# Optimization experiments

Hardware: AMD Instinct MI355X
Metric: run time of the kernel (lower is better)

## Reference

```python
import jax, jax.numpy as jnp
import numpy as np

N = 50000          # nodes
E = 1_600_000      # edges (before self-loops)
F_IN = 256
HID = 32
HEADS = 4
OUT = 64
NEG_SLOPE = 0.2


def setup_inputs() -> dict:
    key = jax.random.key(0)
    ks = jax.random.split(key, 10)
    x = jax.random.normal(ks[0], (N, F_IN), dtype=jnp.float32)
    edge_index = jax.random.randint(ks[1], (2, E), 0, N, dtype=jnp.int64)
    # layer 1: input_dim -> hidden*heads
    W1 = jax.random.normal(ks[2], (F_IN, HEADS * HID), dtype=jnp.float32) / np.sqrt(F_IN)
    att_src1 = jax.random.normal(ks[3], (HEADS, HID), dtype=jnp.float32) / np.sqrt(HID)
    att_dst1 = jax.random.normal(ks[4], (HEADS, HID), dtype=jnp.float32) / np.sqrt(HID)
    b1 = jnp.zeros((HEADS * HID,), dtype=jnp.float32)
    # layer 2: hidden*heads -> out, 1 head, concat=False
    W2 = jax.random.normal(ks[5], (HEADS * HID, OUT), dtype=jnp.float32) / np.sqrt(HEADS * HID)
    att_src2 = jax.random.normal(ks[6], (1, OUT), dtype=jnp.float32) / np.sqrt(OUT)
    att_dst2 = jax.random.normal(ks[7], (1, OUT), dtype=jnp.float32) / np.sqrt(OUT)
    b2 = jnp.zeros((OUT,), dtype=jnp.float32)
    return {"x": x, "edge_index": edge_index, "W1": W1, "att_src1": att_src1,
            "att_dst1": att_dst1, "b1": b1, "W2": W2, "att_src2": att_src2,
            "att_dst2": att_dst2, "b2": b2}


def gat_layer(x, src, dst, W, a_src, a_dst, bias, heads, out_dim, concat):
    n = x.shape[0]
    h = (x @ W).reshape(n, heads, out_dim)              # [N,H,C]
    # per-node attention logits
    al_src = jnp.sum(h * a_src[None], axis=-1)          # [N,H]
    al_dst = jnp.sum(h * a_dst[None], axis=-1)          # [N,H]
    e = al_src[src] + al_dst[dst]                       # [E',H]
    e = jax.nn.leaky_relu(e, NEG_SLOPE)
    # segment softmax over incoming edges of each dst node
    emax = jax.ops.segment_max(e, dst, num_segments=n)  # [N,H]
    ee = jnp.exp(e - emax[dst])
    denom = jax.ops.segment_sum(ee, dst, num_segments=n)
    alpha = ee / denom[dst]                             # [E',H]
    msg = h[src] * alpha[:, :, None]                    # [E',H,C]
    out = jax.ops.segment_sum(msg, dst, num_segments=n)  # [N,H,C]
    if concat:
        out = out.reshape(n, heads * out_dim)
    else:
        out = out.mean(axis=1)
    return out + bias


def reference(x, edge_index, W1, att_src1, att_dst1, b1, W2, att_src2, att_dst2, b2):
    # add self-loops (PyG GATConv default)
    loop = jnp.arange(N, dtype=edge_index.dtype)
    src = jnp.concatenate([edge_index[0], loop])
    dst = jnp.concatenate([edge_index[1], loop])
    # eval mode: dropout(p=0.5) is identity
    h = gat_layer(x, src, dst, W1, att_src1, att_dst1, b1, HEADS, HID, True)
    h = jax.nn.elu(h)
    out = gat_layer(h, src, dst, W2, att_src2, att_dst2, b2, 1, OUT, False)
    return out
```

## Files before the change

kernel.cpp:

```cpp
#include <hip/hip_runtime.h>
#include <hip/hip_bf16.h>
#include <hip/hip_fp16.h>
#include <math.h>

#define NNODES 50000
#define NEDGES 1600000
#define ETOT   (NEDGES + NNODES)
#define F_INN  256
#define NEG_SLOPE 0.2f
#define NBUCK  782
#define BCAP   2624
#define CNBLK  256
#define CBT    1024

__global__ __launch_bounds__(128) void detect_kernel(const unsigned int* __restrict__ ei,
                                                     int* __restrict__ flag) {
    __shared__ int nz;
    if (threadIdx.x == 0) nz = 0;
    __syncthreads();
    unsigned int v = ei[2 * threadIdx.x + 1];
    if (v != 0u) nz = 1;
    __syncthreads();
    if (threadIdx.x == 0) *flag = nz;
}

__device__ __forceinline__ void load_edge(const void* ei, bool is32, int i, int& s, int& d) {
    if (i < NEDGES) {
        if (is32) {
            const int* p = (const int*)ei;
            s = p[i]; d = p[NEDGES + i];
        } else {
            const long long* p = (const long long*)ei;
            s = (int)p[i]; d = (int)p[NEDGES + i];
        }
    } else {
        s = i - NEDGES; d = s;
    }
}

__global__ __launch_bounds__(CBT) void convert_kernel(const void* __restrict__ ei,
                                                      const int* __restrict__ flag,
                                                      int* __restrict__ bcnt,
                                                      int2* __restrict__ bpair) {
    __shared__ int hist[NBUCK];
    __shared__ int base[NBUCK];
    const int t = threadIdx.x;
    const int chunk = (ETOT + CNBLK - 1) / CNBLK;
    const int i0 = blockIdx.x * chunk;
    const int i1 = min(i0 + chunk, ETOT);
    for (int k = t; k < NBUCK; k += CBT) hist[k] = 0;
    __syncthreads();
    const bool is32 = (*flag) != 0;
    for (int i = i0 + t; i < i1; i += CBT) {
        int s, d; load_edge(ei, is32, i, s, d);
        atomicAdd(&hist[d >> 6], 1);
    }
    __syncthreads();
    for (int k = t; k < NBUCK; k += CBT) {
        int c = hist[k];
        base[k] = c ? atomicAdd(&bcnt[k], c) : 0;
        hist[k] = 0;
    }
    __syncthreads();
    for (int i = i0 + t; i < i1; i += CBT) {
        int s, d; load_edge(ei, is32, i, s, d);
        int b = d >> 6;
        int pos = base[b] + atomicAdd(&hist[b], 1);
        bpair[(size_t)b * BCAP + pos] = make_int2(s, d);
    }
}

__global__ __launch_bounds__(256) void deg_kernel(const int2* __restrict__ bpair,
                                                  const int* __restrict__ bcnt,
                                                  int* __restrict__ deg) {
    __shared__ int cnt[64];
    const int b = blockIdx.x, t = threadIdx.x;
    if (t < 64) cnt[t] = 0;
    __syncthreads();
    const int n = bcnt[b];
    const int2* bp = bpair + (size_t)b * BCAP;
    for (int i = t; i < n; i += 256) atomicAdd(&cnt[bp[i].y & 63], 1);
    __syncthreads();
    int node = (b << 6) + t;
    if (t < 64 && node < NNODES) deg[node] = cnt[t];
}

__global__ __launch_bounds__(1024) void scan_kernel(const int* __restrict__ deg,
                                                    int* __restrict__ rowptr) {
    const int CH = 49;
    __shared__ int wsum[16];
    __shared__ int s_total;
    const int tid = threadIdx.x, lane = tid & 63, wid = tid >> 6;
    const int base = tid * CH;
    int sum = 0;
    for (int i = 0; i < CH; ++i) {
        int idx = base + i;
        if (idx < NNODES) sum += deg[idx];
    }
    int v = sum;
    #pragma unroll
    for (int off = 1; off < 64; off <<= 1) {
        int t = __shfl_up(v, off);
        if (lane >= off) v += t;
    }
    if (lane == 63) wsum[wid] = v;
    __syncthreads();
    if (wid == 0) {
        int wv = (lane < 16) ? wsum[lane] : 0;
        #pragma unroll
        for (int off = 1; off < 16; off <<= 1) {
            int t = __shfl_up(wv, off);
            if (lane >= off) wv += t;
        }
        if (lane < 16) wsum[lane] = wv;
        if (lane == 15) s_total = wv;
    }
    __syncthreads();
    int off = (v - sum) + ((wid == 0) ? 0 : wsum[wid - 1]);
    for (int i = 0; i < CH; ++i) {
        int idx = base + i;
        if (idx < NNODES) {
            rowptr[idx] = off;
            off += deg[idx];
        }
    }
    if (tid == 0) rowptr[NNODES] = s_total;
}

__global__ __launch_bounds__(256) void bscatter_kernel(const int2* __restrict__ bpair,
                                                       const int* __restrict__ bcnt,
                                                       const int* __restrict__ rowptr,
                                                       int* __restrict__ ssrc) {
    __shared__ int s_widx[64];
    const int b = blockIdx.x;
    const int t = threadIdx.x;
    const int node0 = b << 6;
    if (t < 64 && node0 + t < NNODES) s_widx[t] = rowptr[node0 + t];
    __syncthreads();
    const int n = bcnt[b];
    const int2* bp = bpair + (size_t)b * BCAP;
    for (int i = t; i < n; i += 256) {
        int2 e = bp[i];
        int pos = atomicAdd(&s_widx[e.y & 63], 1);
        ssrc[pos] = e.x;
    }
}

__global__ __launch_bounds__(256) void gemm1_kernel(const float* __restrict__ x,
                                                    const float* __restrict__ W,
                                                    const float* __restrict__ atts,
                                                    const float* __restrict__ attd,
                                                    __half2* __restrict__ h1h,
                                                    float* __restrict__ als,
                                                    float* __restrict__ ald) {
    __shared__ float xs[32][68];
    __shared__ float ws[32][128];
    const int tid = threadIdx.x;
    const int tx = tid & 15, ty = tid >> 4;
    const int row0 = blockIdx.x * 64;
    float acc[4][8];
    #pragma unroll
    for (int r = 0; r < 4; ++r)
        #pragma unroll
        for (int c = 0; c < 8; ++c) acc[r][c] = 0.f;

    const int lr = tid >> 2;
    const int lk = (tid & 3) * 8;
    const int wk = tid >> 3;
    const int wc = (tid & 7) * 16;

    for (int k0 = 0; k0 < F_INN; k0 += 32) {
        float4 v0 = make_float4(0.f,0.f,0.f,0.f), v1 = v0;
        int gr = row0 + lr;
        if (gr < NNODES) {
            const float* xp = x + (size_t)gr * F_INN + k0 + lk;
            v0 = *(const float4*)xp; v1 = *(const float4*)(xp + 4);
        }
        xs[lk+0][lr]=v0.x; xs[lk+1][lr]=v0.y; xs[lk+2][lr]=v0.z; xs[lk+3][lr]=v0.w;
        xs[lk+4][lr]=v1.x; xs[lk+5][lr]=v1.y; xs[lk+6][lr]=v1.z; xs[lk+7][lr]=v1.w;
        const float* wp = W + (size_t)(k0 + wk) * 128 + wc;
        #pragma unroll
        for (int q = 0; q < 4; ++q)
            *(float4*)&ws[wk][wc + q*4] = *(const float4*)(wp + q*4);
        __syncthreads();
        #pragma unroll
        for (int k = 0; k < 32; ++k) {
            float4 av = *(const float4*)&xs[k][ty*4];
            float4 b0 = *(const float4*)&ws[k][tx*8];
            float4 b1 = *(const float4*)&ws[k][tx*8+4];
            const float a_[4] = {av.x,av.y,av.z,av.w};
            const float b_[8] = {b0.x,b0.y,b0.z,b0.w,b1.x,b1.y,b1.z,b1.w};
            #pragma unroll
            for (int r = 0; r < 4; ++r)
                #pragma unroll
                for (int c = 0; c < 8; ++c)
                    acc[r][c] = fmaf(a_[r], b_[c], acc[r][c]);
        }
        __syncthreads();
    }
    #pragma unroll
    for (int r = 0; r < 4; ++r) {
        int gr = row0 + ty*4 + r;
        bool valid = gr < NNODES;
        float ps = 0.f, pd = 0.f;
        if (valid) {
            float4 pack;
            __half2* pk = (__half2*)&pack;
            pk[0] = __floats2half2_rn(acc[r][0], acc[r][1]);
            pk[1] = __floats2half2_rn(acc[r][2], acc[r][3]);
            pk[2] = __floats2half2_rn(acc[r][4], acc[r][5]);
            pk[3] = __floats2half2_rn(acc[r][6], acc[r][7]);
            *(float4*)(h1h + (size_t)gr*64 + tx*4) = pack;
            #pragma unroll
            for (int c = 0; c < 8; ++c) {
                ps = fmaf(acc[r][c], atts[tx*8 + c], ps);
                pd = fmaf(acc[r][c], attd[tx*8 + c], pd);
            }
        }
        ps += __shfl_xor(ps, 1); ps += __shfl_xor(ps, 2);
        pd += __shfl_xor(pd, 1); pd += __shfl_xor(pd, 2);
        if (valid && (tx & 3) == 0) {
            int hd = tx >> 2;
            als[gr*4 + hd] = ps;
            ald[gr*4 + hd] = pd;
        }
    }
}

__global__ __launch_bounds__(256) void gemm2_kernel(const float* __restrict__ x2,
                                                    const float* __restrict__ W,
                                                    const float* __restrict__ atts,
                                                    const float* __restrict__ attd,
                                                    float* __restrict__ h2,
                                                    float* __restrict__ als,
                                                    float* __restrict__ ald) {
    __shared__ float xs[32][68];
    __shared__ float ws[32][64];
    const int tid = threadIdx.x;
    const int tx = tid & 15, ty = tid >> 4;
    const int row0 = blockIdx.x * 64;
    float acc[4][4];
    #pragma unroll
    for (int r = 0; r < 4; ++r)
        #pragma unroll
        for (int c = 0; c < 4; ++c) acc[r][c] = 0.f;

    const int lr = tid >> 2;
    const int lk = (tid & 3) * 8;
    const int wk = tid >> 3;
    const int wc = (tid & 7) * 8;

    for (int k0 = 0; k0 < 128; k0 += 32) {
        float4 v0 = make_float4(0.f,0.f,0.f,0.f), v1 = v0;
        int gr = row0 + lr;
        if (gr < NNODES) {
            const float* xp = x2 + (size_t)gr * 128 + k0 + lk;
            v0 = *(const float4*)xp; v1 = *(const float4*)(xp + 4);
        }
        xs[lk+0][lr]=v0.x; xs[lk+1][lr]=v0.y; xs[lk+2][lr]=v0.z; xs[lk+3][lr]=v0.w;
        xs[lk+4][lr]=v1.x; xs[lk+5][lr]=v1.y; xs[lk+6][lr]=v1.z; xs[lk+7][lr]=v1.w;
        const float* wp = W + (size_t)(k0 + wk) * 64 + wc;
        *(float4*)&ws[wk][wc]     = *(const float4*)wp;
        *(float4*)&ws[wk][wc + 4] = *(const float4*)(wp + 4);
        __syncthreads();
        #pragma unroll
        for (int k = 0; k < 32; ++k) {
            float4 av = *(const float4*)&xs[k][ty*4];
            float4 bv = *(const float4*)&ws[k][tx*4];
            const float a_[4] = {av.x,av.y,av.z,av.w};
            const float b_[4] = {bv.x,bv.y,bv.z,bv.w};
            #pragma unroll
            for (int r = 0; r < 4; ++r)
                #pragma unroll
                for (int c = 0; c < 4; ++c)
                    acc[r][c] = fmaf(a_[r], b_[c], acc[r][c]);
        }
        __syncthreads();
    }
    #pragma unroll
    for (int r = 0; r < 4; ++r) {
        int gr = row0 + ty*4 + r;
        bool valid = gr < NNODES;
        float ps = 0.f, pd = 0.f;
        if (valid) {
            *(float4*)&h2[(size_t)gr*64 + tx*4] = make_float4(acc[r][0],acc[r][1],acc[r][2],acc[r][3]);
            #pragma unroll
            for (int c = 0; c < 4; ++c) {
                ps = fmaf(acc[r][c], atts[tx*4 + c], ps);
                pd = fmaf(acc[r][c], attd[tx*4 + c], pd);
            }
        }
        ps += __shfl_xor(ps, 1); ps += __shfl_xor(ps, 2);
        ps += __shfl_xor(ps, 4); ps += __shfl_xor(ps, 8);
        pd += __shfl_xor(pd, 1); pd += __shfl_xor(pd, 2);
        pd += __shfl_xor(pd, 4); pd += __shfl_xor(pd, 8);
        if (valid && tx == 0) {
            als[gr] = ps;
            ald[gr] = pd;
        }
    }
}

__device__ __forceinline__ float lrelu(float e) { return e > 0.f ? e : NEG_SLOPE * e; }

__global__ __launch_bounds__(256) void edge1_kernel(const int* __restrict__ rowptr,
                                                    const int* __restrict__ ssrc,
                                                    const float* __restrict__ als,
                                                    const float* __restrict__ ald,
                                                    const __half2* __restrict__ h1h,
                                                    const float* __restrict__ b1,
                                                    float* __restrict__ x2) {
    __shared__ float s_alpha[4][256];
    __shared__ int   s_sidx[4][64];
    __shared__ int   s_nch[4];
    const int lane = threadIdx.x & 63;
    const int wid  = threadIdx.x >> 6;
    const int d = blockIdx.x * 4 + wid;
    const int start = rowptr[d], end = rowptr[d + 1];
    const int deg = end - start;
    float4 aldv = *(const float4*)&ald[d * 4];

    float l0=0.f, l1=0.f, l2=0.f, l3=0.f;
    float4 ex0 = make_float4(0,0,0,0), ex1 = ex0;
    int ss0 = 0, ss1 = 0;
    int it = 0;
    for (int j = start + lane; j < end; j += 64, ++it) {
        int s = ssrc[j];
        float4 a = *(const float4*)&als[s * 4];
        float e0 = __expf(lrelu(a.x + aldv.x));
        float e1 = __expf(lrelu(a.y + aldv.y));
        float e2 = __expf(lrelu(a.z + aldv.z));
        float e3 = __expf(lrelu(a.w + aldv.w));
        if (it == 0)      { ex0 = make_float4(e0,e1,e2,e3); ss0 = s; }
        else if (it == 1) { ex1 = make_float4(e0,e1,e2,e3); ss1 = s; }
        l0 += e0; l1 += e1; l2 += e2; l3 += e3;
    }
    #pragma unroll
    for (int off = 32; off >= 1; off >>= 1) {
        l0 += __shfl_xor(l0, off); l1 += __shfl_xor(l1, off);
        l2 += __shfl_xor(l2, off); l3 += __shfl_xor(l3, off);
    }
    float il0 = 1.f/l0, il1 = 1.f/l1, il2 = 1.f/l2, il3 = 1.f/l3;

    const int nch = (deg + 63) >> 6;
    if (lane == 0) s_nch[wid] = nch;
    __syncthreads();
    const int maxch = max(max(s_nch[0], s_nch[1]), max(s_nch[2], s_nch[3]));

    const int h = lane >> 4;
    float s0 = 0.f, s1 = 0.f;
    for (int c = 0; c < maxch; ++c) {
        const int base = start + c * 64;
        if (c < nch) {
            int j = base + lane;
            if (j < end) {
                int s; float4 ex;
                if (c == 0)      { s = ss0; ex = ex0; }
                else if (c == 1) { s = ss1; ex = ex1; }
                else {
                    s = ssrc[j];
                    float4 a = *(const float4*)&als[s * 4];
                    ex = make_float4(__expf(lrelu(a.x + aldv.x)),
                                     __expf(lrelu(a.y + aldv.y)),
                                     __expf(lrelu(a.z + aldv.z)),
                                     __expf(lrelu(a.w + aldv.w)));
                }
                s_sidx[wid][lane] = s;
                float4 al = make_float4(ex.x*il0, ex.y*il1, ex.z*il2, ex.w*il3);
                *(float4*)&s_alpha[wid][lane * 4] = al;
            }
        }
        __syncthreads();
        if (c < nch) {
            const int cnt = min(64, end - base);
            int jj = 0;
            for (; jj + 3 < cnt; jj += 4) {
                int sA = __builtin_amdgcn_readfirstlane(s_sidx[wid][jj]);
                int sB = __builtin_amdgcn_readfirstlane(s_sidx[wid][jj + 1]);
                int sC = __builtin_amdgcn_readfirstlane(s_sidx[wid][jj + 2]);
                int sD = __builtin_amdgcn_readfirstlane(s_sidx[wid][jj + 3]);
                float aA = s_alpha[wid][jj*4 + h];
                float aB = s_alpha[wid][jj*4 + 4 + h];
                float aC = s_alpha[wid][jj*4 + 8 + h];
                float aD = s_alpha[wid][jj*4 + 12 + h];
                float2 hA = __half22float2(h1h[(size_t)sA * 64 + lane]);
                float2 hB = __half22float2(h1h[(size_t)sB * 64 + lane]);
                float2 hC = __half22float2(h1h[(size_t)sC * 64 + lane]);
                float2 hD = __half22float2(h1h[(size_t)sD * 64 + lane]);
                s0 = fmaf(hA.x, aA, s0); s1 = fmaf(hA.y, aA, s1);
                s0 = fmaf(hB.x, aB, s0); s1 = fmaf(hB.y, aB, s1);
                s0 = fmaf(hC.x, aC, s0); s1 = fmaf(hC.y, aC, s1);
                s0 = fmaf(hD.x, aD, s0); s1 = fmaf(hD.y, aD, s1);
            }
            for (; jj < cnt; ++jj) {
                int sA = __builtin_amdgcn_readfirstlane(s_sidx[wid][jj]);
                float aA = s_alpha[wid][jj*4 + h];
                float2 hA = __half22float2(h1h[(size_t)sA * 64 + lane]);
                s0 = fmaf(hA.x, aA, s0); s1 = fmaf(hA.y, aA, s1);
            }
        }
        __syncthreads();
    }
    const int col = lane << 1;
    float o0 = s0 + b1[col], o1 = s1 + b1[col + 1];
    o0 = o0 > 0.f ? o0 : expm1f(o0);
    o1 = o1 > 0.f ? o1 : expm1f(o1);
    *(float2*)&x2[(size_t)d * 128 + col] = make_float2(o0, o1);
}

__global__ __launch_bounds__(256) void edge2_kernel(const int* __restrict__ rowptr,
                                                    const int* __restrict__ ssrc,
                                                    const float* __restrict__ als,
                                                    const float* __restrict__ ald,
                                                    const float* __restrict__ h2,
                                                    const float* __restrict__ b2,
                                                    float* __restrict__ out) {
    __shared__ float s_alpha[4][64];
    __shared__ int   s_sidx[4][64];
    __shared__ int   s_nch[4];
    const int lane = threadIdx.x & 63;
    const int wid  = threadIdx.x >> 6;
    const int d = blockIdx.x * 4 + wid;
    const int start = rowptr[d], end = rowptr[d + 1];
    const int deg = end - start;
    float aldd = ald[d];

    float l = 0.f;
    float ex0 = 0.f, ex1 = 0.f;
    int ss0 = 0, ss1 = 0;
    int it = 0;
    for (int j = start + lane; j < end; j += 64, ++it) {
        int s = ssrc[j];
        float e = __expf(lrelu(als[s] + aldd));
        if (it == 0)      { ex0 = e; ss0 = s; }
        else if (it == 1) { ex1 = e; ss1 = s; }
        l += e;
    }
    #pragma unroll
    for (int off = 32; off >= 1; off >>= 1) l += __shfl_xor(l, off);
    float invl = 1.f / l;

    const int nch = (deg + 63) >> 6;
    if (lane == 0) s_nch[wid] = nch;
    __syncthreads();
    const int maxch = max(max(s_nch[0], s_nch[1]), max(s_nch[2], s_nch[3]));

    float acc = 0.f;
    for (int c = 0; c < maxch; ++c) {
        const int base = start + c * 64;
        if (c < nch) {
            int j = base + lane;
            if (j < end) {
                int s; float e;
                if (c == 0)      { s = ss0; e = ex0; }
                else if (c == 1) { s = ss1; e = ex1; }
                else { s = ssrc[j]; e = __expf(lrelu(als[s] + aldd)); }
                s_sidx[wid][lane] = s;
                s_alpha[wid][lane] = e * invl;
            }
        }
        __syncthreads();
        if (c < nch) {
            const int cnt = min(64, end - base);
            int jj = 0;
            for (; jj + 3 < cnt; jj += 4) {
                int sA = __builtin_amdgcn_readfirstlane(s_sidx[wid][jj]);
                int sB = __builtin_amdgcn_readfirstlane(s_sidx[wid][jj + 1]);
                int sC = __builtin_amdgcn_readfirstlane(s_sidx[wid][jj + 2]);
                int sD = __builtin_amdgcn_readfirstlane(s_sidx[wid][jj + 3]);
                float aA = s_alpha[wid][jj],     aB = s_alpha[wid][jj + 1];
                float aC = s_alpha[wid][jj + 2], aD = s_alpha[wid][jj + 3];
                float hA = h2[(size_t)sA * 64 + lane];
                float hB = h2[(size_t)sB * 64 + lane];
                float hC = h2[(size_t)sC * 64 + lane];
                float hD = h2[(size_t)sD * 64 + lane];
                acc = fmaf(hA, aA, acc);
                acc = fmaf(hB, aB, acc);
                acc = fmaf(hC, aC, acc);
                acc = fmaf(hD, aD, acc);
            }
            for (; jj < cnt; ++jj) {
                int sA = __builtin_amdgcn_readfirstlane(s_sidx[wid][jj]);
                float aA = s_alpha[wid][jj];
                acc = fmaf(h2[(size_t)sA * 64 + lane], aA, acc);
            }
        }
        __syncthreads();
    }
    out[(size_t)d * 64 + lane] = acc + b2[lane];
}

extern "C" void kernel_launch(void* const* d_in, const int* in_sizes, int n_in,
                              void* d_out, int out_size, void* d_ws, size_t ws_size,
                              hipStream_t stream) {
    const float* x   = (const float*)d_in[0];
    const void*  ei  = d_in[1];
    const float* W1  = (const float*)d_in[2];
    const float* as1 = (const float*)d_in[3];
    const float* ad1 = (const float*)d_in[4];
    const float* b1  = (const float*)d_in[5];
    const float* W2  = (const float*)d_in[6];
    const float* as2 = (const float*)d_in[7];
    const float* ad2 = (const float*)d_in[8];
    const float* b2  = (const float*)d_in[9];
    float* out = (float*)d_out;

    char* p = (char*)d_ws;
    auto alloc = [&](size_t bytes) {
        char* r = p;
        p += (bytes + 255) & ~(size_t)255;
        return r;
    };
    int2*     bpair  = (int2*)alloc(sizeof(int2) * (size_t)NBUCK * BCAP);
    int*      bcnt   = (int*)alloc(sizeof(int) * NBUCK);
    int*      ssrc   = (int*)alloc(sizeof(int) * ETOT);
    int*      deg    = (int*)alloc(sizeof(int) * NNODES);
    int*      rowptr = (int*)alloc(sizeof(int) * (NNODES + 1));
    int*      flag   = (int*)alloc(256);
    float*    als1   = (float*)alloc(sizeof(float) * NNODES * 4);
    float*    ald1   = (float*)alloc(sizeof(float) * NNODES * 4);
    float*    als2v  = (float*)alloc(sizeof(float) * NNODES);
    float*    ald2v  = (float*)alloc(sizeof(float) * NNODES);
    __half2*  h1h    = (__half2*)alloc(sizeof(__half2) * NNODES * 64);
    float*    x2     = (float*)alloc(sizeof(float) * NNODES * 128);
    float*    h2     = (float*)alloc(sizeof(float) * NNODES * 64);

    hipMemsetAsync(bcnt, 0, sizeof(int) * NBUCK, stream);

    detect_kernel<<<1, 128, 0, stream>>>((const unsigned int*)ei, flag);
    convert_kernel<<<CNBLK, CBT, 0, stream>>>(ei, flag, bcnt, bpair);
    deg_kernel<<<NBUCK, 256, 0, stream>>>(bpair, bcnt, deg);
    scan_kernel<<<1, 1024, 0, stream>>>(deg, rowptr);
    bscatter_kernel<<<NBUCK, 256, 0, stream>>>(bpair, bcnt, rowptr, ssrc);
    gemm1_kernel<<<(NNODES + 63) / 64, 256, 0, stream>>>(x, W1, as1, ad1, h1h, als1, ald1);
    edge1_kernel<<<(NNODES + 3) / 4, 256, 0, stream>>>(rowptr, ssrc, als1, ald1, h1h, b1, x2);
    gemm2_kernel<<<(NNODES + 63) / 64, 256, 0, stream>>>(x2, W2, as2, ad2, h2, als2v, ald2v);
    edge2_kernel<<<(NNODES + 3) / 4, 256, 0, stream>>>(rowptr, ssrc, als2v, ald2v, h2, b2, out);
}
```

Baseline: 427.6 us.

## Replace per-node degree scan with bucket-level scan and in-block local scan

Removes the separate degree kernel and the single-block 50k-element scan. A single small kernel now scans the 782 bucket counts, and the scatter kernel counts per-node degrees inside each bucket, does a wavefront scan to produce rowptr, and scatters sources. This drops one launch and a serial single-block pass over all nodes, at the cost of extra counting work in the scatter kernel. It relies on buckets holding contiguous 64-node ranges in order, which the bucketing by d>>6 guarantees.

```diff
diff --git a/kernel.cpp b/kernel.cpp
--- a/kernel.cpp
+++ b/kernel.cpp
@@ -70,75 +70,64 @@
     }
 }
 
-__global__ __launch_bounds__(256) void deg_kernel(const int2* __restrict__ bpair,
-                                                  const int* __restrict__ bcnt,
-                                                  int* __restrict__ deg) {
+__global__ __launch_bounds__(1024) void bucket_scan_kernel(const int* __restrict__ bcnt,
+                                                           int* __restrict__ bbase,
+                                                           int* __restrict__ rowptr) {
+    __shared__ int wsum[16];
+    const int t = threadIdx.x, lane = t & 63, wid = t >> 6;
+    int v = (t < NBUCK) ? bcnt[t] : 0;
+    int incl = v;
+    #pragma unroll
+    for (int off = 1; off < 64; off <<= 1) {
+        int u = __shfl_up(incl, off);
+        if (lane >= off) incl += u;
+    }
+    if (lane == 63) wsum[wid] = incl;
+    __syncthreads();
+    if (wid == 0) {
+        int wv = (lane < 16) ? wsum[lane] : 0;
+        #pragma unroll
+        for (int off = 1; off < 16; off <<= 1) {
+            int u = __shfl_up(wv, off);
+            if (lane >= off) wv += u;
+        }
+        if (lane < 16) wsum[lane] = wv;
+    }
+    __syncthreads();
+    int base = (wid == 0) ? 0 : wsum[wid - 1];
+    if (t < NBUCK) bbase[t] = base + incl - v;
+    if (t == 0) rowptr[NNODES] = ETOT;
+}
+
+__global__ __launch_bounds__(256) void bscatter_kernel(const int2* __restrict__ bpair,
+                                                       const int* __restrict__ bcnt,
+                                                       const int* __restrict__ bbase,
+                                                       int* __restrict__ rowptr,
+                                                       int* __restrict__ ssrc) {
     __shared__ int cnt[64];
-    const int b = blockIdx.x, t = threadIdx.x;
+    __shared__ int s_widx[64];
+    const int b = blockIdx.x;
+    const int t = threadIdx.x;
     if (t < 64) cnt[t] = 0;
     __syncthreads();
     const int n = bcnt[b];
     const int2* bp = bpair + (size_t)b * BCAP;
     for (int i = t; i < n; i += 256) atomicAdd(&cnt[bp[i].y & 63], 1);
     __syncthreads();
-    int node = (b << 6) + t;
-    if (t < 64 && node < NNODES) deg[node] = cnt[t];
-}
-
-__global__ __launch_bounds__(1024) void scan_kernel(const int* __restrict__ deg,
-                                                    int* __restrict__ rowptr) {
-    const int CH = 49;
-    __shared__ int wsum[16];
-    __shared__ int s_total;
-    const int tid = threadIdx.x, lane = tid & 63, wid = tid >> 6;
-    const int base = tid * CH;
-    int sum = 0;
-    for (int i = 0; i < CH; ++i) {
-        int idx = base + i;
-        if (idx < NNODES) sum += deg[idx];
-    }
-    int v = sum;
-    #pragma unroll
-    for (int off = 1; off < 64; off <<= 1) {
-        int t = __shfl_up(v, off);
-        if (lane >= off) v += t;
-    }
-    if (lane == 63) wsum[wid] = v;
-    __syncthreads();
-    if (wid == 0) {
-        int wv = (lane < 16) ? wsum[lane] : 0;
-        #pragma unroll
-        for (int off = 1; off < 16; off <<= 1) {
-            int t = __shfl_up(wv, off);
-            if (lane >= off) wv += t;
-        }
-        if (lane < 16) wsum[lane] = wv;
-        if (lane == 15) s_total = wv;
-    }
-    __syncthreads();
-    int off = (v - sum) + ((wid == 0) ? 0 : wsum[wid - 1]);
-    for (int i = 0; i < CH; ++i) {
-        int idx = base + i;
-        if (idx < NNODES) {
-            rowptr[idx] = off;
-            off += deg[idx];
-        }
-    }
-    if (tid == 0) rowptr[NNODES] = s_total;
-}
-
-__global__ __launch_bounds__(256) void bscatter_kernel(const int2* __restrict__ bpair,
-                                                       const int* __restrict__ bcnt,
-                                                       const int* __restrict__ rowptr,
-                                                       int* __restrict__ ssrc) {
-    __shared__ int s_widx[64];
-    const int b = blockIdx.x;
-    const int t = threadIdx.x;
-    const int node0 = b << 6;
-    if (t < 64 && node0 + t < NNODES) s_widx[t] = rowptr[node0 + t];
-    __syncthreads();
-    const int n = bcnt[b];
-    const int2* bp = bpair + (size_t)b * BCAP;
+    if (t < 64) {
+        int v = cnt[t];
+        int incl = v;
+        #pragma unroll
+        for (int off = 1; off < 64; off <<= 1) {
+            int u = __shfl_up(incl, off);
+            if (t >= off) incl += u;
+        }
+        int excl = bbase[b] + incl - v;
+        int node = (b << 6) + t;
+        if (node < NNODES) rowptr[node] = excl;
+        s_widx[t] = excl;
+    }
+    __syncthreads();
     for (int i = t; i < n; i += 256) {
         int2 e = bp[i];
         int pos = atomicAdd(&s_widx[e.y & 63], 1);
@@ -513,8 +502,8 @@
     };
     int2*     bpair  = (int2*)alloc(sizeof(int2) * (size_t)NBUCK * BCAP);
     int*      bcnt   = (int*)alloc(sizeof(int) * NBUCK);
+    int*      bbase  = (int*)alloc(sizeof(int) * NBUCK);
     int*      ssrc   = (int*)alloc(sizeof(int) * ETOT);
-    int*      deg    = (int*)alloc(sizeof(int) * NNODES);
     int*      rowptr = (int*)alloc(sizeof(int) * (NNODES + 1));
     int*      flag   = (int*)alloc(256);
     float*    als1   = (float*)alloc(sizeof(float) * NNODES * 4);
@@ -529,9 +518,8 @@
 
     detect_kernel<<<1, 128, 0, stream>>>((const unsigned int*)ei, flag);
     convert_kernel<<<CNBLK, CBT, 0, stream>>>(ei, flag, bcnt, bpair);
-    deg_kernel<<<NBUCK, 256, 0, stream>>>(bpair, bcnt, deg);
-    scan_kernel<<<1, 1024, 0, stream>>>(deg, rowptr);
-    bscatter_kernel<<<NBUCK, 256, 0, stream>>>(bpair, bcnt, rowptr, ssrc);
+    bucket_scan_kernel<<<1, 1024, 0, stream>>>(bcnt, bbase, rowptr);
+    bscatter_kernel<<<NBUCK, 256, 0, stream>>>(bpair, bcnt, bbase, rowptr, ssrc);
     gemm1_kernel<<<(NNODES + 63) / 64, 256, 0, stream>>>(x, W1, as1, ad1, h1h, als1, ald1);
     edge1_kernel<<<(NNODES + 3) / 4, 256, 0, stream>>>(rowptr, ssrc, als1, ald1, h1h, b1, x2);
     gemm2_kernel<<<(NNODES + 63) / 64, 256, 0, stream>>>(x2, W2, as2, ad2, h2, als2v, ald2v);
```

Measured after the change: 343.6 us. 1.24x faster.
